# Kernel optimization log

Hardware: AMD Instinct MI355X
Metric: run time of the kernel (lower is better)

The kernel has to match this reference:

```python
import jax, jax.numpy as jnp
import numpy as np

B, S, N, E = 8, 32, 2000, 64000
GH, H = 32, 64  # gat_h, lstm hidden
NEG_SLOPE = 0.2


def setup_inputs() -> dict:
    key = jax.random.key(0)
    ks = jax.random.split(key, 12)
    f32 = jnp.float32
    x = jax.random.normal(ks[0], (B, S, N), f32)
    edge_index = jax.random.randint(ks[1], (2, E), 0, N)
    # GATConv(1, GH, heads=1, concat=False): lin weight [GH,1] -> vector, att_src/att_dst [GH], bias [GH]
    w_lin = jax.random.normal(ks[2], (GH,), f32)
    att_src = jax.random.normal(ks[3], (GH,), f32) * 0.1
    att_dst = jax.random.normal(ks[4], (GH,), f32) * 0.1
    gat_bias = jax.random.normal(ks[5], (GH,), f32) * 0.01
    D = GH * N  # LSTM input size
    W_ih = jax.random.normal(ks[6], (4 * H, D), f32) * (1.0 / np.sqrt(D))
    W_hh = jax.random.normal(ks[7], (4 * H, H), f32) * (1.0 / np.sqrt(H))
    b_ih = jax.random.normal(ks[8], (4 * H,), f32) * 0.01
    b_hh = jax.random.normal(ks[9], (4 * H,), f32) * 0.01
    W_head = jax.random.normal(ks[10], (N, H), f32) * (1.0 / np.sqrt(H))
    b_head = jax.random.normal(ks[11], (N,), f32) * 0.01
    return {"x": x, "edge_index": edge_index, "w_lin": w_lin, "att_src": att_src,
            "att_dst": att_dst, "gat_bias": gat_bias, "W_ih": W_ih, "W_hh": W_hh,
            "b_ih": b_ih, "b_hh": b_hh, "W_head": W_head, "b_head": b_head}


def reference(x, edge_index, w_lin, att_src, att_dst, gat_bias,
              W_ih, W_hh, b_ih, b_hh, W_head, b_head):
    x = x.astype(jnp.float32)
    # --- GAT (in_channels=1, heads=1), batched over (B,S) ---
    # PyG default: add self-loops
    loops = jnp.arange(N)
    ei = jnp.concatenate([edge_index, jnp.stack([loops, loops])], axis=1)
    src, dst = ei[0], ei[1]  # [Et], Et = E + N
    # lifted feature h_n = x_n * w_lin (rank-1), so attention logits are scalar per node
    a_src = x * jnp.dot(w_lin, att_src)  # [B,S,N]
    a_dst = x * jnp.dot(w_lin, att_dst)  # [B,S,N]
    e = jax.nn.leaky_relu(a_src[..., src] + a_dst[..., dst], NEG_SLOPE)  # [B,S,Et]
    e = jnp.moveaxis(e, -1, 0)  # [Et,B,S] (segment axis leading)
    seg_max = jax.ops.segment_max(e, dst, num_segments=N)  # [N,B,S]
    e = jnp.exp(e - seg_max[dst])
    denom = jax.ops.segment_sum(e, dst, num_segments=N)  # [N,B,S]
    alpha = e / denom[dst]  # edge softmax over incoming edges
    x_src = jnp.moveaxis(x[..., src], -1, 0)  # [Et,B,S]
    agg = jax.ops.segment_sum(alpha * x_src, dst, num_segments=N)  # [N,B,S]
    agg = jnp.moveaxis(agg, 0, -1)  # [B,S,N]
    # outer product with w_lin restores [.,GH]; add bias, then relu (from forward)
    h = jax.nn.relu(agg[..., None] * w_lin + gat_bias)  # [B,S,N,GH]
    lstm_in = h.reshape(B, S, N * GH)

    # --- LSTM (1 layer, batch_first), keep final hidden state ---
    def step(carry, xt):
        hp, cp = carry
        gates = xt @ W_ih.T + b_ih + hp @ W_hh.T + b_hh  # [B,4H]
        i, f, g, o = jnp.split(gates, 4, axis=-1)
        c = jax.nn.sigmoid(f) * cp + jax.nn.sigmoid(i) * jnp.tanh(g)
        hn = jax.nn.sigmoid(o) * jnp.tanh(c)
        return (hn, c), None

    h0 = jnp.zeros((B, H), jnp.float32)
    c0 = jnp.zeros((B, H), jnp.float32)
    (hT, _), _ = jax.lax.scan(step, (h0, c0), jnp.swapaxes(lstm_in, 0, 1))
    return hT @ W_head.T + b_head  # [B,N]
```

## Files before the change

### kernel.cpp

```cpp
#include <hip/hip_runtime.h>
#include <hip/hip_bf16.h>
#include <cstddef>
#include <cstdint>

#define B_  8
#define S_  32
#define BT_ 256
#define N_  2000
#define E_  64000
#define GH_ 32
#define H_  64
#define G4_ 256
#define D_  64000
#define NEG_SLOPE_ 0.2f

#define KC_   125
#define NPC_  16

typedef __attribute__((ext_vector_type(8))) short short8;
typedef __attribute__((ext_vector_type(4))) float floatx4;
union U8 { uint32_t u[4]; short8 s; };

__device__ __forceinline__ float fsigmoid(float x) { return 1.0f / (1.0f + __expf(-x)); }
__device__ __forceinline__ float ftanh_(float x)   { return 1.0f - 2.0f / (__expf(2.0f * x) + 1.0f); }

__device__ __forceinline__ void split2(float v0, float v1, uint32_t& hi, uint32_t& lo) {
  uint32_t b0 = __float_as_uint(v0), b1 = __float_as_uint(v1);
  uint32_t h0 = b0 & 0xffff0000u,    h1 = b1 & 0xffff0000u;
  hi = (b0 >> 16) | h1;
  float l0 = v0 - __uint_as_float(h0);
  float l1 = v1 - __uint_as_float(h1);
  lo = (__float_as_uint(l0) >> 16) | (__float_as_uint(l1) & 0xffff0000u);
}


__global__ __launch_bounds__(256) void hist_kernel(
    const int* __restrict__ ei, int* __restrict__ deg)
{
  const int i = blockIdx.x * 256 + threadIdx.x;
  if (i < E_) atomicAdd(&deg[ei[E_ + i]], 1);
}

__global__ __launch_bounds__(256) void scan_kernel(
    const int* __restrict__ deg, int* __restrict__ rowptr, int* __restrict__ cursor)
{
  __shared__ int tsum[256];
  const int tid = threadIdx.x;
  int v[8];
  int s = 0;
  const int base = tid * 8;
#pragma unroll
  for (int j = 0; j < 8; ++j) {
    const int idx = base + j;
    const int d = (idx < N_) ? deg[idx] : 0;
    v[j] = s;
    s += d;
  }
  tsum[tid] = s;
  __syncthreads();
  for (int off = 1; off < 256; off <<= 1) {
    int t = 0;
    if (tid >= off) t = tsum[tid - off];
    __syncthreads();
    tsum[tid] += t;
    __syncthreads();
  }
  const int ebase = tsum[tid] - s;
#pragma unroll
  for (int j = 0; j < 8; ++j) {
    const int idx = base + j;
    if (idx < N_) {
      const int r = ebase + v[j];
      rowptr[idx] = r;
      cursor[idx] = r;
    }
  }
  if (tid == 0) rowptr[N_] = E_;
}

__global__ __launch_bounds__(256) void scatter_kernel(
    const int* __restrict__ ei, int* __restrict__ cursor, int* __restrict__ csr_src)
{
  const int i = blockIdx.x * 256 + threadIdx.x;
  if (i >= E_) return;
  const int s = ei[i];
  const int d = ei[E_ + i];
  const int pos = atomicAdd(&cursor[d], 1);
  csr_src[pos] = s;
}

__global__ __launch_bounds__(256) void transpose_kernel(
    const float* __restrict__ x, float* __restrict__ xT)
{
  __shared__ float tile[32][33];
  const int tx = threadIdx.x & 31;
  const int ty = threadIdx.x >> 5;
  const int n0  = blockIdx.x * 32;
  const int bt0 = blockIdx.y * 32;
#pragma unroll
  for (int r = 0; r < 4; ++r) {
    const int bt = bt0 + ty + r * 8;
    const int nn = n0 + tx;
    if (nn < N_) tile[ty + r * 8][tx] = x[(size_t)bt * N_ + nn];
  }
  __syncthreads();
#pragma unroll
  for (int r = 0; r < 4; ++r) {
    const int n = n0 + ty + r * 8;
    if (n < N_) xT[(size_t)n * BT_ + bt0 + tx] = tile[tx][ty + r * 8];
  }
}

__global__ __launch_bounds__(256) void gat_gather_kernel(
    const float* __restrict__ xT, const int* __restrict__ rowptr,
    const int* __restrict__ csr_src,
    const float* __restrict__ w_lin, const float* __restrict__ att_src,
    const float* __restrict__ att_dst, float* __restrict__ agg_T)
{
  __shared__ int srcs[512];
  const int n   = blockIdx.x;
  const int tid = threadIdx.x;

  float c_s = 0.f, c_d = 0.f;
  for (int g = 0; g < GH_; ++g) {
    const float w = w_lin[g];
    c_s += w * att_src[g];
    c_d += w * att_dst[g];
  }

  const int r0 = rowptr[n];
  const int r1 = rowptr[n + 1];
  const int d  = r1 - r0;
  for (int i = tid; i < d && i < 512; i += 256) srcs[i] = csr_src[r0 + i];
  __syncthreads();

  const float xn = xT[(size_t)n * BT_ + tid];
  float e = (c_s + c_d) * xn;
  e = e > 0.f ? e : NEG_SLOPE_ * e;
  float w = __expf(e);
  float num = w * xn;
  float den = w;

  for (int p = 0; p < d; ++p) {
    int s;
    if (p < 512) s = srcs[p]; else s = csr_src[r0 + p];
    const float xs = xT[(size_t)s * BT_ + tid];
    float ee = c_s * xs + c_d * xn;
    ee = ee > 0.f ? ee : NEG_SLOPE_ * ee;
    const float ww = __expf(ee);
    num += ww * xs;
    den += ww;
  }
  agg_T[(size_t)n * BT_ + tid] = num / den;
}

__global__ __launch_bounds__(256) void gate_mfma_kernel(
    const float* __restrict__ W_ih, const float* __restrict__ agg_T,
    const float* __restrict__ w_lin, const float* __restrict__ gat_bias,
    float* __restrict__ partial, float* __restrict__ pre_gates, int use_atomic)
{
  __shared__ float agg_s[NPC_ * 256];

  const int tid  = threadIdx.x;
  const int nb   = blockIdx.x;
  const int kc   = blockIdx.y;
  const int n0   = kc * NPC_;
  const int wv   = tid >> 6;
  const int lane = tid & 63;
  const int i16  = lane & 15;
  const int q    = lane >> 4;
  const int jw   = nb * 64 + wv * 16;

  {
    const float4* src = (const float4*)(agg_T + (size_t)n0 * 256);
    float4* dst = (float4*)agg_s;
#pragma unroll
    for (int p = 0; p < 4; ++p) dst[tid + p * 256] = src[tid + p * 256];
  }

  float wlr[8], gbr[8];
#pragma unroll
  for (int j = 0; j < 8; ++j) {
    wlr[j] = w_lin[q * 8 + j];
    gbr[j] = gat_bias[q * 8 + j];
  }

  floatx4 acc[16];
#pragma unroll
  for (int mt = 0; mt < 16; ++mt)
#pragma unroll
    for (int r = 0; r < 4; ++r) acc[mt][r] = 0.f;

  __syncthreads();

  const float* Wrow = W_ih + (size_t)(jw + i16) * D_ + (size_t)n0 * GH_ + q * 8;

  float4 cb0 = *(const float4*)(Wrow);
  float4 cb1 = *(const float4*)(Wrow + 4);

#pragma unroll 1
  for (int nn = 0; nn < NPC_; ++nn) {
    const int nnx = (nn + 1) & (NPC_ - 1);
    float4 pb0 = *(const float4*)(Wrow + nnx * GH_);
    float4 pb1 = *(const float4*)(Wrow + nnx * GH_ + 4);

    short8 bh, bl;
    {
      U8 Hh, Ll;
      split2(cb0.x, cb0.y, Hh.u[0], Ll.u[0]);
      split2(cb0.z, cb0.w, Hh.u[1], Ll.u[1]);
      split2(cb1.x, cb1.y, Hh.u[2], Ll.u[2]);
      split2(cb1.z, cb1.w, Hh.u[3], Ll.u[3]);
      bh = Hh.s; bl = Ll.s;
    }

#pragma unroll
    for (int mt = 0; mt < 16; ++mt) {
      const float a = agg_s[nn * 256 + mt * 16 + i16];
      U8 Ah, Al;
#pragma unroll
      for (int p = 0; p < 4; ++p) {
        float v0 = fmaf(a, wlr[2 * p],     gbr[2 * p]);
        float v1 = fmaf(a, wlr[2 * p + 1], gbr[2 * p + 1]);
        v0 = fmaxf(v0, 0.f);
        v1 = fmaxf(v1, 0.f);
        split2(v0, v1, Ah.u[p], Al.u[p]);
      }
      acc[mt] = __builtin_amdgcn_mfma_f32_16x16x32_bf16(Ah.s, bh, acc[mt], 0, 0, 0);
      acc[mt] = __builtin_amdgcn_mfma_f32_16x16x32_bf16(Al.s, bh, acc[mt], 0, 0, 0);
      acc[mt] = __builtin_amdgcn_mfma_f32_16x16x32_bf16(Ah.s, bl, acc[mt], 0, 0, 0);
    }
    cb0 = pb0; cb1 = pb1;
  }

  const int j = jw + i16;
#pragma unroll
  for (int mt = 0; mt < 16; ++mt) {
    const int bt = mt * 16 + q * 4;
    if (use_atomic) {
#pragma unroll
      for (int r = 0; r < 4; ++r) atomicAdd(&pre_gates[(bt + r) * G4_ + j], acc[mt][r]);
    } else {
#pragma unroll
      for (int r = 0; r < 4; ++r)
        partial[((size_t)kc * 256 + (bt + r)) * 256 + j] = acc[mt][r];
    }
  }
}

__global__ __launch_bounds__(256) void reduce_kernel(
    const float* __restrict__ partial, float* __restrict__ pre_gates)
{
  const int o = blockIdx.x * 256 + threadIdx.x;
  float s0 = 0.f, s1 = 0.f, s2 = 0.f, s3 = 0.f;
  int kc = 0;
  for (; kc + 4 <= KC_; kc += 4) {
    s0 += partial[(size_t)(kc + 0) * 65536 + o];
    s1 += partial[(size_t)(kc + 1) * 65536 + o];
    s2 += partial[(size_t)(kc + 2) * 65536 + o];
    s3 += partial[(size_t)(kc + 3) * 65536 + o];
  }
  for (; kc < KC_; ++kc) s0 += partial[(size_t)kc * 65536 + o];
  pre_gates[o] = (s0 + s1) + (s2 + s3);
}

__global__ __launch_bounds__(256) void lstm_kernel(
    const float* __restrict__ pre_gates, const float* __restrict__ W_hh,
    const float* __restrict__ b_ih, const float* __restrict__ b_hh,
    float* __restrict__ hT)
{
  const int b   = blockIdx.x;
  const int tid = threadIdx.x;
  __shared__ float h_s[H_];
  __shared__ float g_s[G4_];

  float wr[H_];
#pragma unroll
  for (int k = 0; k < H_; ++k) wr[k] = W_hh[(size_t)tid * H_ + k];

  float pg[S_];
#pragma unroll
  for (int t = 0; t < S_; ++t) pg[t] = pre_gates[(size_t)(b * S_ + t) * G4_ + tid];

  const float bias = b_ih[tid] + b_hh[tid];
  if (tid < H_) h_s[tid] = 0.f;
  float c = 0.f;
  __syncthreads();

  for (int t = 0; t < S_; ++t) {
    float g0 = pg[t] + bias, g1 = 0.f, g2 = 0.f, g3 = 0.f;
#pragma unroll
    for (int k = 0; k < H_; k += 4) {
      g0 = fmaf(wr[k + 0], h_s[k + 0], g0);
      g1 = fmaf(wr[k + 1], h_s[k + 1], g1);
      g2 = fmaf(wr[k + 2], h_s[k + 2], g2);
      g3 = fmaf(wr[k + 3], h_s[k + 3], g3);
    }
    g_s[tid] = (g0 + g1) + (g2 + g3);
    __syncthreads();
    if (tid < H_) {
      const float ig = fsigmoid(g_s[tid]);
      const float fg = fsigmoid(g_s[H_ + tid]);
      const float gg = ftanh_(g_s[2 * H_ + tid]);
      const float og = fsigmoid(g_s[3 * H_ + tid]);
      c = fg * c + ig * gg;
      h_s[tid] = og * ftanh_(c);
    }
    __syncthreads();
  }
  if (tid < H_) hT[b * H_ + tid] = h_s[tid];
}

__global__ __launch_bounds__(256) void head_kernel(
    const float* __restrict__ hT, const float* __restrict__ W_head,
    const float* __restrict__ b_head, float* __restrict__ out)
{
  const int o = blockIdx.x * 256 + threadIdx.x;
  if (o >= B_ * N_) return;
  const int b = o / N_;
  const int n = o - b * N_;
  const float4* w4 = (const float4*)(W_head + (size_t)n * H_);
  const float4* h4 = (const float4*)(hT + (size_t)b * H_);
  float acc = b_head[n];
#pragma unroll
  for (int q = 0; q < H_ / 4; ++q) {
    const float4 w = w4[q];
    const float4 h = h4[q];
    acc += w.x * h.x + w.y * h.y + w.z * h.z + w.w * h.w;
  }
  out[o] = acc;
}

extern "C" void kernel_launch(void* const* d_in, const int* in_sizes, int n_in,
                              void* d_out, int out_size, void* d_ws, size_t ws_size,
                              hipStream_t stream) {
  const float* x        = (const float*)d_in[0];
  const int*   ei       = (const int*)  d_in[1];
  const float* w_lin    = (const float*)d_in[2];
  const float* att_src  = (const float*)d_in[3];
  const float* att_dst  = (const float*)d_in[4];
  const float* gat_bias = (const float*)d_in[5];
  const float* W_ih     = (const float*)d_in[6];
  const float* W_hh     = (const float*)d_in[7];
  const float* b_ih     = (const float*)d_in[8];
  const float* b_hh     = (const float*)d_in[9];
  const float* W_head   = (const float*)d_in[10];
  const float* b_head   = (const float*)d_in[11];
  float* out = (float*)d_out;

  char* ws = (char*)d_ws;
  float* agg_T     = (float*)(ws + 0);
  float* pre_gates = (float*)(ws + 2048000);
  float* hT        = (float*)(ws + 2310144);
  float* xT        = (float*)(ws + 2312192);
  int*   deg       = (int*)  (ws + 4360192);
  int*   rowptr    = (int*)  (ws + 4368384);
  int*   cursor    = (int*)  (ws + 4376576);
  int*   csr_src   = (int*)  (ws + 4384768);
  float* partial   = (float*)(ws + 4640768);
  const size_t need = 4640768 + (size_t)KC_ * 65536 * sizeof(float);
  const int use_atomic = (ws_size < need) ? 1 : 0;

  hipMemsetAsync(deg, 0, N_ * sizeof(int), stream);
  hist_kernel<<<dim3((E_ + 255) / 256), dim3(256), 0, stream>>>(ei, deg);
  scan_kernel<<<dim3(1), dim3(256), 0, stream>>>(deg, rowptr, cursor);
  scatter_kernel<<<dim3((E_ + 255) / 256), dim3(256), 0, stream>>>(ei, cursor, csr_src);
  transpose_kernel<<<dim3((N_ + 31) / 32, BT_ / 32), dim3(256), 0, stream>>>(x, xT);
  gat_gather_kernel<<<dim3(N_), dim3(256), 0, stream>>>(
      xT, rowptr, csr_src, w_lin, att_src, att_dst, agg_T);

  if (use_atomic) {
    hipMemsetAsync(pre_gates, 0, G4_ * BT_ * sizeof(float), stream);
  }
  gate_mfma_kernel<<<dim3(4, KC_), dim3(256), 0, stream>>>(
      W_ih, agg_T, w_lin, gat_bias, partial, pre_gates, use_atomic);
  if (!use_atomic) {
    reduce_kernel<<<dim3(256), dim3(256), 0, stream>>>(partial, pre_gates);
  }

  lstm_kernel<<<dim3(B_), dim3(256), 0, stream>>>(pre_gates, W_hh, b_ih, b_hh, hT);
  head_kernel<<<dim3((B_ * N_ + 255) / 256), dim3(256), 0, stream>>>(hT, W_head, b_head, out);
}
```

Measured before the change: 250.1 us.

## Retile gate MFMA kernel so waves share W_ih columns and split bt rows

Each wave in the gate GEMM kernel now covers 64 bt rows against all 64 output columns of the block, instead of 256 rows against its own 16 columns. Each W_ih element is loaded once per block and its bf16 split is amortised over four M tiles, while the activation split work drops from 16 to 4 tiles per wave. The hi/lo bf16 packing also uses a byte-permute builtin in place of shift/or. The prefetch of the next W chunk is removed, so load latency is less hidden, and four row streams per lane are loaded each iteration.

Result: faster. 225.2 us (-10.0%).

```diff
diff --git a/kernel.cpp b/kernel.cpp
--- a/kernel.cpp
+++ b/kernel.cpp
@@ -26,11 +26,10 @@
 
 __device__ __forceinline__ void split2(float v0, float v1, uint32_t& hi, uint32_t& lo) {
   uint32_t b0 = __float_as_uint(v0), b1 = __float_as_uint(v1);
-  uint32_t h0 = b0 & 0xffff0000u,    h1 = b1 & 0xffff0000u;
-  hi = (b0 >> 16) | h1;
-  float l0 = v0 - __uint_as_float(h0);
-  float l1 = v1 - __uint_as_float(h1);
-  lo = (__float_as_uint(l0) >> 16) | (__float_as_uint(l1) & 0xffff0000u);
+  hi = __builtin_amdgcn_perm(b1, b0, 0x07060302u);
+  float l0 = v0 - __uint_as_float(b0 & 0xffff0000u);
+  float l1 = v1 - __uint_as_float(b1 & 0xffff0000u);
+  lo = __builtin_amdgcn_perm(__float_as_uint(l1), __float_as_uint(l0), 0x07060302u);
 }
 
 
@@ -169,7 +168,7 @@
   const int lane = tid & 63;
   const int i16  = lane & 15;
   const int q    = lane >> 4;
-  const int jw   = nb * 64 + wv * 16;
+  const int j0   = nb * 64;
 
   {
     const float4* src = (const float4*)(agg_T + (size_t)n0 * 256);
@@ -180,70 +179,84 @@
 
   float wlr[8], gbr[8];
 #pragma unroll
-  for (int j = 0; j < 8; ++j) {
-    wlr[j] = w_lin[q * 8 + j];
-    gbr[j] = gat_bias[q * 8 + j];
-  }
-
-  floatx4 acc[16];
-#pragma unroll
-  for (int mt = 0; mt < 16; ++mt)
-#pragma unroll
-    for (int r = 0; r < 4; ++r) acc[mt][r] = 0.f;
-
-  __syncthreads();
-
-  const float* Wrow = W_ih + (size_t)(jw + i16) * D_ + (size_t)n0 * GH_ + q * 8;
-
-  float4 cb0 = *(const float4*)(Wrow);
-  float4 cb1 = *(const float4*)(Wrow + 4);
+  for (int jx = 0; jx < 8; ++jx) {
+    wlr[jx] = w_lin[q * 8 + jx];
+    gbr[jx] = gat_bias[q * 8 + jx];
+  }
+
+  floatx4 acc[4][4];
+#pragma unroll
+  for (int mt = 0; mt < 4; ++mt)
+#pragma unroll
+    for (int jt = 0; jt < 4; ++jt)
+#pragma unroll
+      for (int r = 0; r < 4; ++r) acc[mt][jt][r] = 0.f;
+
+  __syncthreads();
+
+  const float* Wr0 = W_ih + (size_t)(j0 +  0 + i16) * D_ + (size_t)n0 * GH_ + q * 8;
+  const float* Wr1 = W_ih + (size_t)(j0 + 16 + i16) * D_ + (size_t)n0 * GH_ + q * 8;
+  const float* Wr2 = W_ih + (size_t)(j0 + 32 + i16) * D_ + (size_t)n0 * GH_ + q * 8;
+  const float* Wr3 = W_ih + (size_t)(j0 + 48 + i16) * D_ + (size_t)n0 * GH_ + q * 8;
 
 #pragma unroll 1
   for (int nn = 0; nn < NPC_; ++nn) {
-    const int nnx = (nn + 1) & (NPC_ - 1);
-    float4 pb0 = *(const float4*)(Wrow + nnx * GH_);
-    float4 pb1 = *(const float4*)(Wrow + nnx * GH_ + 4);
-
-    short8 bh, bl;
-    {
+    float4 b0[4], b1[4];
+    b0[0] = *(const float4*)(Wr0 + nn * GH_);     b1[0] = *(const float4*)(Wr0 + nn * GH_ + 4);
+    b0[1] = *(const float4*)(Wr1 + nn * GH_);     b1[1] = *(const float4*)(Wr1 + nn * GH_ + 4);
+    b0[2] = *(const float4*)(Wr2 + nn * GH_);     b1[2] = *(const float4*)(Wr2 + nn * GH_ + 4);
+    b0[3] = *(const float4*)(Wr3 + nn * GH_);     b1[3] = *(const float4*)(Wr3 + nn * GH_ + 4);
+
+    short8 ah[4], al[4];
+#pragma unroll
+    for (int mt = 0; mt < 4; ++mt) {
+      const float a = agg_s[nn * 256 + wv * 64 + mt * 16 + i16];
       U8 Hh, Ll;
-      split2(cb0.x, cb0.y, Hh.u[0], Ll.u[0]);
-      split2(cb0.z, cb0.w, Hh.u[1], Ll.u[1]);
-      split2(cb1.x, cb1.y, Hh.u[2], Ll.u[2]);
-      split2(cb1.z, cb1.w, Hh.u[3], Ll.u[3]);
-      bh = Hh.s; bl = Ll.s;
-    }
-
-#pragma unroll
-    for (int mt = 0; mt < 16; ++mt) {
-      const float a = agg_s[nn * 256 + mt * 16 + i16];
-      U8 Ah, Al;
 #pragma unroll
       for (int p = 0; p < 4; ++p) {
         float v0 = fmaf(a, wlr[2 * p],     gbr[2 * p]);
         float v1 = fmaf(a, wlr[2 * p + 1], gbr[2 * p + 1]);
         v0 = fmaxf(v0, 0.f);
         v1 = fmaxf(v1, 0.f);
-        split2(v0, v1, Ah.u[p], Al.u[p]);
+        split2(v0, v1, Hh.u[p], Ll.u[p]);
       }
-      acc[mt] = __builtin_amdgcn_mfma_f32_16x16x32_bf16(Ah.s, bh, acc[mt], 0, 0, 0);
-      acc[mt] = __builtin_amdgcn_mfma_f32_16x16x32_bf16(Al.s, bh, acc[mt], 0, 0, 0);
-      acc[mt] = __builtin_amdgcn_mfma_f32_16x16x32_bf16(Ah.s, bl, acc[mt], 0, 0, 0);
-    }
-    cb0 = pb0; cb1 = pb1;
-  }
-
-  const int j = jw + i16;
-#pragma unroll
-  for (int mt = 0; mt < 16; ++mt) {
-    const int bt = mt * 16 + q * 4;
-    if (use_atomic) {
-#pragma unroll
-      for (int r = 0; r < 4; ++r) atomicAdd(&pre_gates[(bt + r) * G4_ + j], acc[mt][r]);
-    } else {
-#pragma unroll
-      for (int r = 0; r < 4; ++r)
-        partial[((size_t)kc * 256 + (bt + r)) * 256 + j] = acc[mt][r];
+      ah[mt] = Hh.s; al[mt] = Ll.s;
+    }
+
+#pragma unroll
+    for (int jt = 0; jt < 4; ++jt) {
+      short8 bh, bl;
+      {
+        U8 Hh, Ll;
+        split2(b0[jt].x, b0[jt].y, Hh.u[0], Ll.u[0]);
+        split2(b0[jt].z, b0[jt].w, Hh.u[1], Ll.u[1]);
+        split2(b1[jt].x, b1[jt].y, Hh.u[2], Ll.u[2]);
+        split2(b1[jt].z, b1[jt].w, Hh.u[3], Ll.u[3]);
+        bh = Hh.s; bl = Ll.s;
+      }
+#pragma unroll
+      for (int mt = 0; mt < 4; ++mt) {
+        acc[mt][jt] = __builtin_amdgcn_mfma_f32_16x16x32_bf16(ah[mt], bh, acc[mt][jt], 0, 0, 0);
+        acc[mt][jt] = __builtin_amdgcn_mfma_f32_16x16x32_bf16(al[mt], bh, acc[mt][jt], 0, 0, 0);
+        acc[mt][jt] = __builtin_amdgcn_mfma_f32_16x16x32_bf16(ah[mt], bl, acc[mt][jt], 0, 0, 0);
+      }
+    }
+  }
+
+#pragma unroll
+  for (int mt = 0; mt < 4; ++mt) {
+    const int bt = wv * 64 + mt * 16 + q * 4;
+#pragma unroll
+    for (int jt = 0; jt < 4; ++jt) {
+      const int j = j0 + jt * 16 + i16;
+      if (use_atomic) {
+#pragma unroll
+        for (int r = 0; r < 4; ++r) atomicAdd(&pre_gates[(bt + r) * G4_ + j], acc[mt][jt][r]);
+      } else {
+#pragma unroll
+        for (int r = 0; r < 4; ++r)
+          partial[((size_t)kc * 256 + (bt + r)) * 256 + j] = acc[mt][jt][r];
+      }
     }
   }
 }
```
